# Optimization experiments

Measured on AMD Instinct MI355X. Metric: run time of the kernel, lower is better.

The kernel has to match this reference:

```python
import jax, jax.numpy as jnp
import numpy as np

N = 8192      # num nodes
IN = 256      # in_channels
HID = 128     # hidden_channels
DEG = 32      # avg degree
E = N * DEG   # num edges (without self loops)
EPS_NORM = 1e-12
EPS_SOFTMAX = 1e-16


def setup_inputs() -> dict:
    key = jax.random.key(0)
    ks = jax.random.split(key, 8)
    x = jax.random.normal(ks[0], (N, IN), jnp.float32)
    # random sparse graph with no self loops (PyG AGNNConv removes then re-adds them)
    dst = jax.random.randint(ks[1], (E,), 0, N)
    off = jax.random.randint(ks[2], (E,), 1, N)
    src = (dst + off) % N
    edge_index = jnp.stack([src, dst]).astype(jnp.int32)  # [2, E]
    adj = jnp.zeros((N, N), jnp.float32).at[src, dst].set(1.0)  # dense H used in final mm
    s1 = 1.0 / np.sqrt(IN)
    s2 = 1.0 / np.sqrt(HID)
    W1 = jax.random.uniform(ks[3], (HID, IN), jnp.float32, -s1, s1)
    b1 = jax.random.uniform(ks[4], (HID,), jnp.float32, -s1, s1)
    W2 = jax.random.uniform(ks[5], (HID, HID), jnp.float32, -s2, s2)
    b2 = jax.random.uniform(ks[6], (HID,), jnp.float32, -s2, s2)
    beta2 = jnp.ones((1,), jnp.float32)  # learnable beta of prop2 (init 1.0)
    return dict(x=x, adj=adj, edge_index=edge_index, W1=W1, b1=b1, W2=W2, b2=b2, beta2=beta2)


def _agnn(x, src, dst, beta):
    # L2 normalize (F.normalize, eps=1e-12)
    norm = jnp.sqrt(jnp.sum(x * x, axis=-1, keepdims=True))
    xn = x / jnp.maximum(norm, EPS_NORM)
    # cosine-similarity attention score per edge, scaled by beta
    alpha = beta * jnp.sum(xn[src] * xn[dst], axis=-1)        # [E']
    # softmax over edges grouped by destination node (PyG softmax)
    m = jax.ops.segment_max(alpha, dst, num_segments=N)       # [N]
    e = jnp.exp(alpha - m[dst])
    s = jax.ops.segment_sum(e, dst, num_segments=N)           # [N]
    w = e / (s[dst] + EPS_SOFTMAX)                            # [E']
    # scatter-add weighted source features
    return jax.ops.segment_sum(x[src] * w[:, None], dst, num_segments=N)


def reference(x, adj, edge_index, W1, b1, W2, b2, beta2):
    # eval mode: dropout(p=0.5) is identity
    h = jax.nn.relu(x @ W1.T + b1)                            # [N, HID]
    # add self loops (edge_index is guaranteed self-loop free)
    loops = jnp.arange(N, dtype=edge_index.dtype)
    src = jnp.concatenate([edge_index[0], loops])
    dst = jnp.concatenate([edge_index[1], loops])
    h = _agnn(h, src, dst, jnp.float32(1.0))                  # prop1: fixed beta=1
    h = _agnn(h, src, dst, beta2[0])                          # prop2: learnable beta
    h = jax.nn.relu(h @ W2.T + b2)                            # [N, HID]
    return adj @ h                                            # torch.mm(H, x)
```

## Files before the change

kernel.cpp:

```cpp
#include <hip/hip_runtime.h>
#include <stdint.h>

typedef unsigned long long u64;

#define IN_C 256
#define HID_C 128
#define SRC_CAP 192
#define MM_CAP 256

__device__ __align__(256) unsigned char g_fallback[28u << 20];

__global__ void k_zero128(uint4* __restrict__ p, int n16) {
  int i = blockIdx.x * blockDim.x + threadIdx.x;
  int stride = gridDim.x * blockDim.x;
  uint4 z = make_uint4(0u, 0u, 0u, 0u);
  for (; i < n16; i += stride) p[i] = z;
}

__device__ inline void gemm_body(int bid, int tid,
                                 const float* __restrict__ X, const float* __restrict__ W,
                                 const float* __restrict__ b, float* __restrict__ C, int K,
                                 float* __restrict__ ssq_out, float* __restrict__ invn_out,
                                 float (*Ws)[HID_C + 4], float (*Xs)[64]) {
  const int rl = tid >> 5;
  const int cg = tid & 31;
  const int row0 = bid * 16;
  float4 acc0 = make_float4(0.f, 0.f, 0.f, 0.f);
  float4 acc1 = make_float4(0.f, 0.f, 0.f, 0.f);
  for (int kt = 0; kt < K; kt += 64) {
    for (int idx = tid; idx < HID_C * 16; idx += 256) {
      int c = idx >> 4, kq = idx & 15;
      const float4 w4 = *(const float4*)&W[c * K + kt + kq * 4];
      Ws[kq * 4 + 0][c] = w4.x;
      Ws[kq * 4 + 1][c] = w4.y;
      Ws[kq * 4 + 2][c] = w4.z;
      Ws[kq * 4 + 3][c] = w4.w;
    }
    {
      int r = tid >> 4, kq = tid & 15;
      const float4 x4 = *(const float4*)&X[(row0 + r) * K + kt + kq * 4];
      *(float4*)&Xs[r][kq * 4] = x4;
    }
    __syncthreads();
#pragma unroll 16
    for (int kk = 0; kk < 64; ++kk) {
      const float4 w = *(const float4*)&Ws[kk][cg * 4];
      const float x0 = Xs[rl * 2 + 0][kk];
      const float x1 = Xs[rl * 2 + 1][kk];
      acc0.x = fmaf(w.x, x0, acc0.x); acc0.y = fmaf(w.y, x0, acc0.y);
      acc0.z = fmaf(w.z, x0, acc0.z); acc0.w = fmaf(w.w, x0, acc0.w);
      acc1.x = fmaf(w.x, x1, acc1.x); acc1.y = fmaf(w.y, x1, acc1.y);
      acc1.z = fmaf(w.z, x1, acc1.z); acc1.w = fmaf(w.w, x1, acc1.w);
    }
    __syncthreads();
  }
  const float4 bb = *(const float4*)&b[cg * 4];
  float4 o0, o1;
  o0.x = fmaxf(acc0.x + bb.x, 0.f); o0.y = fmaxf(acc0.y + bb.y, 0.f);
  o0.z = fmaxf(acc0.z + bb.z, 0.f); o0.w = fmaxf(acc0.w + bb.w, 0.f);
  o1.x = fmaxf(acc1.x + bb.x, 0.f); o1.y = fmaxf(acc1.y + bb.y, 0.f);
  o1.z = fmaxf(acc1.z + bb.z, 0.f); o1.w = fmaxf(acc1.w + bb.w, 0.f);
  int r0 = row0 + rl * 2;
  *(float4*)&C[r0 * HID_C + cg * 4] = o0;
  *(float4*)&C[(r0 + 1) * HID_C + cg * 4] = o1;
  if (ssq_out) {
    float s0 = o0.x * o0.x + o0.y * o0.y + o0.z * o0.z + o0.w * o0.w;
    float s1 = o1.x * o1.x + o1.y * o1.y + o1.z * o1.z + o1.w * o1.w;
#pragma unroll
    for (int off = 16; off >= 1; off >>= 1) {
      s0 += __shfl_xor(s0, off, 64);
      s1 += __shfl_xor(s1, off, 64);
    }
    if (cg == 0) {
      ssq_out[r0] = s0;
      ssq_out[r0 + 1] = s1;
      invn_out[r0] = 1.0f / fmaxf(sqrtf(s0), 1e-12f);
      invn_out[r0 + 1] = 1.0f / fmaxf(sqrtf(s1), 1e-12f);
    }
  }
}

__global__ __launch_bounds__(256) void k_build_gemm(
    const float* __restrict__ X, const float* __restrict__ W, const float* __restrict__ b,
    float* __restrict__ C, int K, float* __restrict__ ssq_out, float* __restrict__ invn_out,
    int nblk_gemm,
    const int* __restrict__ src, const int* __restrict__ dst, int E,
    u64* __restrict__ bmT, u64* __restrict__ bmS, int wpr,
    u64* __restrict__ duplist, int* __restrict__ dupcnt, int dupcap) {
  __shared__ float Ws[64][HID_C + 4];
  __shared__ float Xs[16][64];
  if ((int)blockIdx.x < nblk_gemm) {
    gemm_body(blockIdx.x, threadIdx.x, X, W, b, C, K, ssq_out, invn_out, Ws, Xs);
    return;
  }
  int e = (blockIdx.x - nblk_gemm) * 256 + threadIdx.x;
  if (e < E) {
    int s = src[e], d = dst[e];
    u64 bit = 1ull << (s & 63);
    u64 old = atomicOr(&bmT[(size_t)d * wpr + (s >> 6)], bit);
    if (old & bit) {
      int i = atomicAdd(dupcnt, 1);
      if (i < dupcap) duplist[i] = ((u64)(uint32_t)d << 32) | (uint32_t)s;
    }
    atomicOr(&bmS[(size_t)s * wpr + (d >> 6)], 1ull << (d & 63));
  }
}

__global__ __launch_bounds__(256) void k_gemm_relu(
    const float* __restrict__ X, const float* __restrict__ W,
    const float* __restrict__ b, float* __restrict__ C, int K,
    float* __restrict__ ssq_out, float* __restrict__ invn_out) {
  __shared__ float Ws[64][HID_C + 4];
  __shared__ float Xs[16][64];
  gemm_body(blockIdx.x, threadIdx.x, X, W, b, C, K, ssq_out, invn_out, Ws, Xs);
}

__global__ void k_agg(const float* __restrict__ hin, float* __restrict__ hout,
                      const u64* __restrict__ bmT, int wpr,
                      const u64* __restrict__ duplist, const int* __restrict__ dupcnt, int dupcap,
                      const float* __restrict__ invn, const float* __restrict__ ssq,
                      const float* __restrict__ beta_ptr,
                      float* __restrict__ ssq_out, float* __restrict__ invn_out,
                      int n) {
  __shared__ int   s_src[4][SRC_CAP];
  __shared__ float s_wt[4][SRC_CAP];
  int wv = threadIdx.x >> 6;
  int wid = (blockIdx.x * blockDim.x + threadIdx.x) >> 6;
  int lane = threadIdx.x & 63;
  if (wid >= n) return;
  int* S = s_src[wv];
  float* WT = s_wt[wv];

  const u64* row = bmT + (size_t)wid * wpr;
  u64 w0 = row[lane];
  u64 w1 = row[64 + lane];
  int c = __popcll(w0) + __popcll(w1);
  int incl = c;
#pragma unroll
  for (int off = 1; off < 64; off <<= 1) {
    int v = __shfl_up(incl, off, 64);
    if (lane >= off) incl += v;
  }
  int M = __shfl(incl, 63, 64);
  int pos = incl - c;
  u64 t = w0;
  while (t) {
    int bp = __ffsll(t) - 1; t &= t - 1;
    if (pos < SRC_CAP) S[pos] = (lane << 6) + bp;
    pos++;
  }
  t = w1;
  while (t) {
    int bp = __ffsll(t) - 1; t &= t - 1;
    if (pos < SRC_CAP) S[pos] = ((64 + lane) << 6) + bp;
    pos++;
  }
  if (M > SRC_CAP) M = SRC_CAP;

  int D = min(*dupcnt, dupcap);
  for (int base = 0; base < D; base += 64) {
    int m = min(64, D - base);
    bool match = false; int sE = 0x7fffffff;
    if (lane < m) {
      u64 ent = duplist[base + lane];
      if ((int)(ent >> 32) == wid) { match = true; sE = (int)(uint32_t)ent; }
    }
    while (__ballot(match)) {
      int sv = match ? sE : 0x7fffffff;
#pragma unroll
      for (int o = 32; o >= 1; o >>= 1) sv = min(sv, __shfl_xor(sv, o, 64));
      int cnt = (int)__popcll(__ballot(match && sE == sv));
      if (lane < cnt && M + lane < SRC_CAP) S[M + lane] = sv;
      M = min(M + cnt, SRC_CAP);
      if (match && sE == sv) match = false;
    }
  }

  float beta = beta_ptr ? beta_ptr[0] : 1.0f;
  float invd = invn[wid];
  float eloop = __expf(beta * (ssq[wid] * invd) * invd);

  const int g = lane >> 4;
  const int gl = lane & 15;
  const float* qrow = &hin[wid * HID_C + gl * 8];
  float4 qa = *(const float4*)&qrow[0];
  float4 qb = *(const float4*)&qrow[4];
  float esum = 0.f;
  for (int e0 = 0; e0 < M; e0 += 4) {
    int e = e0 + g;
    bool valid = (e < M);
    int s = S[valid ? e : e0];
    const float* r = &hin[s * HID_C + gl * 8];
    float4 ra = *(const float4*)&r[0];
    float4 rb = *(const float4*)&r[4];
    float d = qa.x * ra.x + qa.y * ra.y + qa.z * ra.z + qa.w * ra.w +
              qb.x * rb.x + qb.y * rb.y + qb.z * rb.z + qb.w * rb.w;
#pragma unroll
    for (int off = 1; off <= 8; off <<= 1) d += __shfl_xor(d, off, 64);
    float iv = invn[s];
    float w = valid ? __expf(beta * d * invd * iv) : 0.f;
    esum += w;
    if (gl == 0 && valid) WT[e] = w;
  }
  esum += __shfl_xor(esum, 16, 64);
  esum += __shfl_xor(esum, 32, 64);
  float ssum = eloop + esum;

  float2 hd = *(const float2*)&hin[wid * HID_C + lane * 2];
  float2 acc = make_float2(eloop * hd.x, eloop * hd.y);
  int e2 = 0;
  for (; e2 + 1 < M; e2 += 2) {
    float wa = WT[e2], wb = WT[e2 + 1];
    int sa = S[e2], sb = S[e2 + 1];
    float2 ha = *(const float2*)&hin[sa * HID_C + lane * 2];
    float2 hb = *(const float2*)&hin[sb * HID_C + lane * 2];
    acc.x = fmaf(wa, ha.x, acc.x); acc.y = fmaf(wa, ha.y, acc.y);
    acc.x = fmaf(wb, hb.x, acc.x); acc.y = fmaf(wb, hb.y, acc.y);
  }
  if (e2 < M) {
    float wa = WT[e2];
    int sa = S[e2];
    float2 ha = *(const float2*)&hin[sa * HID_C + lane * 2];
    acc.x = fmaf(wa, ha.x, acc.x); acc.y = fmaf(wa, ha.y, acc.y);
  }
  float winv = 1.0f / (ssum + 1e-16f);
  acc.x *= winv; acc.y *= winv;
  *(float2*)&hout[wid * HID_C + lane * 2] = acc;
  if (ssq_out) {
    float s = acc.x * acc.x + acc.y * acc.y;
#pragma unroll
    for (int off = 32; off >= 1; off >>= 1) s += __shfl_xor(s, off, 64);
    if (lane == 0) {
      ssq_out[wid] = s;
      invn_out[wid] = 1.0f / fmaxf(sqrtf(s), 1e-12f);
    }
  }
}

__global__ void k_mm_bits(const u64* __restrict__ bm, const float* __restrict__ h,
                          float* __restrict__ out, int n, int wpr) {
  __shared__ int s_idx[4][MM_CAP];
  int wv = threadIdx.x >> 6;
  int wid = (blockIdx.x * blockDim.x + threadIdx.x) >> 6;
  int lane = threadIdx.x & 63;
  if (wid >= n) return;
  int* S = s_idx[wv];
  const u64* row = bm + (size_t)wid * wpr;
  u64 w0 = row[lane];
  u64 w1 = row[64 + lane];
  int c = __popcll(w0) + __popcll(w1);
  int incl = c;
#pragma unroll
  for (int off = 1; off < 64; off <<= 1) {
    int v = __shfl_up(incl, off, 64);
    if (lane >= off) incl += v;
  }
  int M = __shfl(incl, 63, 64);
  int pos = incl - c;
  u64 t = w0;
  while (t) {
    int bp = __ffsll(t) - 1; t &= t - 1;
    if (pos < MM_CAP) S[pos] = (lane << 6) + bp;
    pos++;
  }
  t = w1;
  while (t) {
    int bp = __ffsll(t) - 1; t &= t - 1;
    if (pos < MM_CAP) S[pos] = ((64 + lane) << 6) + bp;
    pos++;
  }
  if (M > MM_CAP) M = MM_CAP;
  float2 acc = make_float2(0.f, 0.f);
  int i = 0;
  for (; i + 1 < M; i += 2) {
    int ka = S[i], kb = S[i + 1];
    float2 ha = *(const float2*)&h[ka * HID_C + lane * 2];
    float2 hb = *(const float2*)&h[kb * HID_C + lane * 2];
    acc.x += ha.x + hb.x;
    acc.y += ha.y + hb.y;
  }
  if (i < M) {
    float2 ha = *(const float2*)&h[S[i] * HID_C + lane * 2];
    acc.x += ha.x;
    acc.y += ha.y;
  }
  *(float2*)&out[wid * HID_C + lane * 2] = acc;
}

extern "C" void kernel_launch(void* const* d_in, const int* in_sizes, int n_in,
                              void* d_out, int out_size, void* d_ws, size_t ws_size,
                              hipStream_t stream) {
  const float* x     = (const float*)d_in[0];
  const int*   eio   = (const int*)d_in[2];
  const float* W1    = (const float*)d_in[3];
  const float* b1    = (const float*)d_in[4];
  const float* W2    = (const float*)d_in[5];
  const float* b2    = (const float*)d_in[6];
  const float* beta2 = (const float*)d_in[7];
  float* out = (float*)d_out;

  const int N = in_sizes[0] / IN_C;
  const int E = in_sizes[2] / 2;
  const int WPR = N / 64;
  const int* esrc = eio;
  const int* edst = eio + E;
  const int DUPCAP = E;

  size_t off = 0;
  auto take = [&](size_t bytes) -> size_t {
    size_t o = off;
    off = (off + bytes + 255) & ~(size_t)255;
    return o;
  };
  size_t o_bufA   = take((size_t)N * HID_C * 4);
  size_t o_bufB   = take((size_t)N * HID_C * 4);
  size_t o_invnA  = take((size_t)N * 4);
  size_t o_ssqA   = take((size_t)N * 4);
  size_t o_invnB  = take((size_t)N * 4);
  size_t o_ssqB   = take((size_t)N * 4);
  size_t o_bmT    = take((size_t)N * WPR * 8);
  size_t o_bmS    = take((size_t)N * WPR * 8);
  size_t o_dupcnt = take(256);
  size_t need_zero_end = o_dupcnt + 256;
  size_t o_duplist = take((size_t)DUPCAP * 8);
  size_t need_full = off;

  unsigned char* base = (unsigned char*)d_ws;
  if (ws_size < need_full) {
    void* p = nullptr;
    hipGetSymbolAddress(&p, HIP_SYMBOL(g_fallback));
    base = (unsigned char*)p;
  }

  float* bufA    = (float*)(base + o_bufA);
  float* bufB    = (float*)(base + o_bufB);
  float* invnA   = (float*)(base + o_invnA);
  float* ssqA    = (float*)(base + o_ssqA);
  float* invnB   = (float*)(base + o_invnB);
  float* ssqB    = (float*)(base + o_ssqB);
  u64*   bmT     = (u64*)(base + o_bmT);
  u64*   bmS     = (u64*)(base + o_bmS);
  int*   dupcnt  = (int*)(base + o_dupcnt);
  u64*   duplist = (u64*)(base + o_duplist);

  dim3 blk(256);

  {
    size_t zbytes = need_zero_end - o_bmT;
    int n16 = (int)(zbytes / 16);
    k_zero128<<<dim3(4096), blk, 0, stream>>>((uint4*)(base + o_bmT), n16);
  }

  {
    int nblk_gemm = N / 16;
    int nblk_build = (E + 255) / 256;
    k_build_gemm<<<dim3(nblk_gemm + nblk_build), blk, 0, stream>>>(
        x, W1, b1, bufA, IN_C, ssqA, invnA, nblk_gemm,
        esrc, edst, E, bmT, bmS, WPR, duplist, dupcnt, DUPCAP);
  }

  k_agg<<<dim3(N / 4), blk, 0, stream>>>(bufA, bufB, bmT, WPR, duplist, dupcnt, DUPCAP,
                                         invnA, ssqA, nullptr, ssqB, invnB, N);

  k_agg<<<dim3(N / 4), blk, 0, stream>>>(bufB, bufA, bmT, WPR, duplist, dupcnt, DUPCAP,
                                         invnB, ssqB, beta2, nullptr, nullptr, N);

  k_gemm_relu<<<dim3(N / 16), blk, 0, stream>>>(bufA, W2, b2, bufB, HID_C, nullptr, nullptr);

  k_mm_bits<<<dim3(N / 4), blk, 0, stream>>>(bmS, bufB, out, N, WPR);
}
```

Measured before the change: 128.0 us.

## Fuse attention weight and aggregation passes; cache neighbor lists between AGNN layers

The aggregation kernel now accumulates the weighted source features in the same loop that computes attention scores. It reuses the source rows already loaded for the dot product instead of storing weights to shared memory and re-gathering rows in a second pass. The first propagation also writes the enumerated neighbor list and degree to global memory, so the second propagation reads them back instead of redoing the bitmap scan and duplicate-list search. The cost is extra cross-group shuffle reductions for eight accumulators, more registers, and a larger workspace.

New measurement: 110.4 us. -13.8%, faster.

```diff
diff --git a/kernel.cpp b/kernel.cpp
--- a/kernel.cpp
+++ b/kernel.cpp
@@ -8,7 +8,7 @@
 #define SRC_CAP 192
 #define MM_CAP 256
 
-__device__ __align__(256) unsigned char g_fallback[28u << 20];
+__device__ __align__(256) unsigned char g_fallback[40u << 20];
 
 __global__ void k_zero128(uint4* __restrict__ p, int n16) {
   int i = blockIdx.x * blockDim.x + threadIdx.x;
@@ -118,62 +118,68 @@
 __global__ void k_agg(const float* __restrict__ hin, float* __restrict__ hout,
                       const u64* __restrict__ bmT, int wpr,
                       const u64* __restrict__ duplist, const int* __restrict__ dupcnt, int dupcap,
+                      int* __restrict__ glist, int* __restrict__ gdeg, int enumerate,
                       const float* __restrict__ invn, const float* __restrict__ ssq,
                       const float* __restrict__ beta_ptr,
                       float* __restrict__ ssq_out, float* __restrict__ invn_out,
                       int n) {
-  __shared__ int   s_src[4][SRC_CAP];
-  __shared__ float s_wt[4][SRC_CAP];
+  __shared__ int s_src[4][SRC_CAP];
   int wv = threadIdx.x >> 6;
   int wid = (blockIdx.x * blockDim.x + threadIdx.x) >> 6;
   int lane = threadIdx.x & 63;
   if (wid >= n) return;
   int* S = s_src[wv];
-  float* WT = s_wt[wv];
-
-  const u64* row = bmT + (size_t)wid * wpr;
-  u64 w0 = row[lane];
-  u64 w1 = row[64 + lane];
-  int c = __popcll(w0) + __popcll(w1);
-  int incl = c;
-#pragma unroll
-  for (int off = 1; off < 64; off <<= 1) {
-    int v = __shfl_up(incl, off, 64);
-    if (lane >= off) incl += v;
-  }
-  int M = __shfl(incl, 63, 64);
-  int pos = incl - c;
-  u64 t = w0;
-  while (t) {
-    int bp = __ffsll(t) - 1; t &= t - 1;
-    if (pos < SRC_CAP) S[pos] = (lane << 6) + bp;
-    pos++;
-  }
-  t = w1;
-  while (t) {
-    int bp = __ffsll(t) - 1; t &= t - 1;
-    if (pos < SRC_CAP) S[pos] = ((64 + lane) << 6) + bp;
-    pos++;
-  }
-  if (M > SRC_CAP) M = SRC_CAP;
-
-  int D = min(*dupcnt, dupcap);
-  for (int base = 0; base < D; base += 64) {
-    int m = min(64, D - base);
-    bool match = false; int sE = 0x7fffffff;
-    if (lane < m) {
-      u64 ent = duplist[base + lane];
-      if ((int)(ent >> 32) == wid) { match = true; sE = (int)(uint32_t)ent; }
-    }
-    while (__ballot(match)) {
-      int sv = match ? sE : 0x7fffffff;
-#pragma unroll
-      for (int o = 32; o >= 1; o >>= 1) sv = min(sv, __shfl_xor(sv, o, 64));
-      int cnt = (int)__popcll(__ballot(match && sE == sv));
-      if (lane < cnt && M + lane < SRC_CAP) S[M + lane] = sv;
-      M = min(M + cnt, SRC_CAP);
-      if (match && sE == sv) match = false;
-    }
+  int M;
+
+  if (enumerate) {
+    const u64* row = bmT + (size_t)wid * wpr;
+    u64 w0 = row[lane];
+    u64 w1 = row[64 + lane];
+    int c = __popcll(w0) + __popcll(w1);
+    int incl = c;
+#pragma unroll
+    for (int off = 1; off < 64; off <<= 1) {
+      int v = __shfl_up(incl, off, 64);
+      if (lane >= off) incl += v;
+    }
+    M = __shfl(incl, 63, 64);
+    int pos = incl - c;
+    u64 t = w0;
+    while (t) {
+      int bp = __ffsll(t) - 1; t &= t - 1;
+      if (pos < SRC_CAP) S[pos] = (lane << 6) + bp;
+      pos++;
+    }
+    t = w1;
+    while (t) {
+      int bp = __ffsll(t) - 1; t &= t - 1;
+      if (pos < SRC_CAP) S[pos] = ((64 + lane) << 6) + bp;
+      pos++;
+    }
+    if (M > SRC_CAP) M = SRC_CAP;
+    int D = min(*dupcnt, dupcap);
+    for (int base = 0; base < D; base += 64) {
+      int m = min(64, D - base);
+      bool match = false; int sE = 0x7fffffff;
+      if (lane < m) {
+        u64 ent = duplist[base + lane];
+        if ((int)(ent >> 32) == wid) { match = true; sE = (int)(uint32_t)ent; }
+      }
+      while (__ballot(match)) {
+        int sv = match ? sE : 0x7fffffff;
+#pragma unroll
+        for (int o = 32; o >= 1; o >>= 1) sv = min(sv, __shfl_xor(sv, o, 64));
+        int cnt = (int)__popcll(__ballot(match && sE == sv));
+        if (lane < cnt && M + lane < SRC_CAP) S[M + lane] = sv;
+        M = min(M + cnt, SRC_CAP);
+        if (match && sE == sv) match = false;
+      }
+    }
+    for (int i = lane; i < M; i += 64) glist[wid * SRC_CAP + i] = S[i];
+    if (lane == 0) gdeg[wid] = M;
+  } else {
+    M = gdeg[wid];
+    for (int i = lane; i < M; i += 64) S[i] = glist[wid * SRC_CAP + i];
   }
 
   float beta = beta_ptr ? beta_ptr[0] : 1.0f;
@@ -185,7 +191,17 @@
   const float* qrow = &hin[wid * HID_C + gl * 8];
   float4 qa = *(const float4*)&qrow[0];
   float4 qb = *(const float4*)&qrow[4];
-  float esum = 0.f;
+  float4 A0, A1;
+  float esum;
+  if (g == 0) {
+    A0 = make_float4(eloop * qa.x, eloop * qa.y, eloop * qa.z, eloop * qa.w);
+    A1 = make_float4(eloop * qb.x, eloop * qb.y, eloop * qb.z, eloop * qb.w);
+    esum = eloop;
+  } else {
+    A0 = make_float4(0.f, 0.f, 0.f, 0.f);
+    A1 = make_float4(0.f, 0.f, 0.f, 0.f);
+    esum = 0.f;
+  }
   for (int e0 = 0; e0 < M; e0 += 4) {
     int e = e0 + g;
     bool valid = (e < M);
@@ -197,42 +213,37 @@
               qb.x * rb.x + qb.y * rb.y + qb.z * rb.z + qb.w * rb.w;
 #pragma unroll
     for (int off = 1; off <= 8; off <<= 1) d += __shfl_xor(d, off, 64);
-    float iv = invn[s];
-    float w = valid ? __expf(beta * d * invd * iv) : 0.f;
+    float w = valid ? __expf(beta * d * invd * invn[s]) : 0.f;
     esum += w;
-    if (gl == 0 && valid) WT[e] = w;
-  }
-  esum += __shfl_xor(esum, 16, 64);
-  esum += __shfl_xor(esum, 32, 64);
-  float ssum = eloop + esum;
-
-  float2 hd = *(const float2*)&hin[wid * HID_C + lane * 2];
-  float2 acc = make_float2(eloop * hd.x, eloop * hd.y);
-  int e2 = 0;
-  for (; e2 + 1 < M; e2 += 2) {
-    float wa = WT[e2], wb = WT[e2 + 1];
-    int sa = S[e2], sb = S[e2 + 1];
-    float2 ha = *(const float2*)&hin[sa * HID_C + lane * 2];
-    float2 hb = *(const float2*)&hin[sb * HID_C + lane * 2];
-    acc.x = fmaf(wa, ha.x, acc.x); acc.y = fmaf(wa, ha.y, acc.y);
-    acc.x = fmaf(wb, hb.x, acc.x); acc.y = fmaf(wb, hb.y, acc.y);
-  }
-  if (e2 < M) {
-    float wa = WT[e2];
-    int sa = S[e2];
-    float2 ha = *(const float2*)&hin[sa * HID_C + lane * 2];
-    acc.x = fmaf(wa, ha.x, acc.x); acc.y = fmaf(wa, ha.y, acc.y);
-  }
-  float winv = 1.0f / (ssum + 1e-16f);
-  acc.x *= winv; acc.y *= winv;
-  *(float2*)&hout[wid * HID_C + lane * 2] = acc;
-  if (ssq_out) {
-    float s = acc.x * acc.x + acc.y * acc.y;
-#pragma unroll
-    for (int off = 32; off >= 1; off >>= 1) s += __shfl_xor(s, off, 64);
-    if (lane == 0) {
-      ssq_out[wid] = s;
-      invn_out[wid] = 1.0f / fmaxf(sqrtf(s), 1e-12f);
+    A0.x = fmaf(w, ra.x, A0.x); A0.y = fmaf(w, ra.y, A0.y);
+    A0.z = fmaf(w, ra.z, A0.z); A0.w = fmaf(w, ra.w, A0.w);
+    A1.x = fmaf(w, rb.x, A1.x); A1.y = fmaf(w, rb.y, A1.y);
+    A1.z = fmaf(w, rb.z, A1.z); A1.w = fmaf(w, rb.w, A1.w);
+  }
+#pragma unroll
+  for (int off = 16; off <= 32; off <<= 1) {
+    esum += __shfl_xor(esum, off, 64);
+    A0.x += __shfl_xor(A0.x, off, 64); A0.y += __shfl_xor(A0.y, off, 64);
+    A0.z += __shfl_xor(A0.z, off, 64); A0.w += __shfl_xor(A0.w, off, 64);
+    A1.x += __shfl_xor(A1.x, off, 64); A1.y += __shfl_xor(A1.y, off, 64);
+    A1.z += __shfl_xor(A1.z, off, 64); A1.w += __shfl_xor(A1.w, off, 64);
+  }
+  float winv = 1.0f / (esum + 1e-16f);
+  A0.x *= winv; A0.y *= winv; A0.z *= winv; A0.w *= winv;
+  A1.x *= winv; A1.y *= winv; A1.z *= winv; A1.w *= winv;
+  if (g == 0) {
+    float* orow = &hout[wid * HID_C + gl * 8];
+    *(float4*)&orow[0] = A0;
+    *(float4*)&orow[4] = A1;
+    if (ssq_out) {
+      float s = A0.x * A0.x + A0.y * A0.y + A0.z * A0.z + A0.w * A0.w +
+                A1.x * A1.x + A1.y * A1.y + A1.z * A1.z + A1.w * A1.w;
+#pragma unroll
+      for (int off = 1; off <= 8; off <<= 1) s += __shfl_xor(s, off, 64);
+      if (gl == 0) {
+        ssq_out[wid] = s;
+        invn_out[wid] = 1.0f / fmaxf(sqrtf(s), 1e-12f);
+      }
     }
   }
 }
@@ -318,6 +329,8 @@
   size_t o_ssqA   = take((size_t)N * 4);
   size_t o_invnB  = take((size_t)N * 4);
   size_t o_ssqB   = take((size_t)N * 4);
+  size_t o_glist  = take((size_t)N * SRC_CAP * 4);
+  size_t o_gdeg   = take((size_t)N * 4);
   size_t o_bmT    = take((size_t)N * WPR * 8);
   size_t o_bmS    = take((size_t)N * WPR * 8);
   size_t o_dupcnt = take(256);
@@ -338,6 +351,8 @@
   float* ssqA    = (float*)(base + o_ssqA);
   float* invnB   = (float*)(base + o_invnB);
   float* ssqB    = (float*)(base + o_ssqB);
+  int*   glist   = (int*)(base + o_glist);
+  int*   gdeg    = (int*)(base + o_gdeg);
   u64*   bmT     = (u64*)(base + o_bmT);
   u64*   bmS     = (u64*)(base + o_bmS);
   int*   dupcnt  = (int*)(base + o_dupcnt);
@@ -360,9 +375,11 @@
   }
 
   k_agg<<<dim3(N / 4), blk, 0, stream>>>(bufA, bufB, bmT, WPR, duplist, dupcnt, DUPCAP,
+                                         glist, gdeg, 1,
                                          invnA, ssqA, nullptr, ssqB, invnB, N);
 
   k_agg<<<dim3(N / 4), blk, 0, stream>>>(bufB, bufA, bmT, WPR, duplist, dupcnt, DUPCAP,
+                                         glist, gdeg, 0,
                                          invnB, ssqB, beta2, nullptr, nullptr, N);
 
   k_gemm_relu<<<dim3(N / 16), blk, 0, stream>>>(bufA, W2, b2, bufB, HID_C, nullptr, nullptr);
```
